# Performance work log

Measured on AMD Instinct MI355X. Metric: run time of the kernel, lower is better.

## Reference

```python
import jax, jax.numpy as jnp
import numpy as np

N = 100000      # nodes
E = 1600000     # edges (before self-loops)
F_IN = 128      # num_node_features
H = 8           # heads in conv1
C = 16          # per-head channels in conv1 (hard-coded in module)
K = 32          # num_classes (conv2 out, single head)
NEG_SLOPE = 0.2 # PyG GATConv default


def setup_inputs() -> dict:
    key = jax.random.key(0)
    ks = jax.random.split(key, 8)
    x = jax.random.normal(ks[0], (N, F_IN), dtype=jnp.float32)
    edge_index = jax.random.randint(ks[1], (2, E), 0, N, dtype=jnp.int32)
    # conv1 params (Glorot-ish scale)
    W1 = jax.random.normal(ks[2], (H * C, F_IN), dtype=jnp.float32) / np.sqrt(F_IN)
    att_src1 = jax.random.normal(ks[3], (H, C), dtype=jnp.float32) / np.sqrt(C)
    att_dst1 = jax.random.normal(ks[4], (H, C), dtype=jnp.float32) / np.sqrt(C)
    b1 = jnp.zeros((H * C,), dtype=jnp.float32)
    # conv2 params (heads=1)
    W2 = jax.random.normal(ks[5], (K, H * C), dtype=jnp.float32) / np.sqrt(H * C)
    att_src2 = jax.random.normal(ks[6], (1, K), dtype=jnp.float32) / np.sqrt(K)
    att_dst2 = jax.random.normal(ks[7], (1, K), dtype=jnp.float32) / np.sqrt(K)
    b2 = jnp.zeros((K,), dtype=jnp.float32)
    return {"inputs": x, "edge_index": edge_index,
            "W1": W1, "att_src1": att_src1, "att_dst1": att_dst1, "b1": b1,
            "W2": W2, "att_src2": att_src2, "att_dst2": att_dst2, "b2": b2}


def gat_conv(x, src, dst, W, a_src, a_dst, bias, heads, ch):
    # x: [N, F_in]; src/dst: [E2] (self-loops already appended)
    h = (x @ W.T).reshape(N, heads, ch)                  # [N, H, C]
    al_s = (h * a_src[None]).sum(-1)                     # [N, H]
    al_d = (h * a_dst[None]).sum(-1)                     # [N, H]
    e = al_s[src] + al_d[dst]                            # [E2, H]
    e = jnp.where(e >= 0, e, NEG_SLOPE * e)              # LeakyReLU
    # segment softmax over edges sharing a destination node
    m = jax.ops.segment_max(e, dst, num_segments=N)      # [N, H]
    p = jnp.exp(e - m[dst])
    s = jax.ops.segment_sum(p, dst, num_segments=N)
    alpha = p / (s[dst] + 1e-16)                         # [E2, H]
    msg = h[src] * alpha[:, :, None]                     # [E2, H, C]
    out = jax.ops.segment_sum(msg, dst, num_segments=N)  # [N, H, C]
    return out.reshape(N, heads * ch) + bias, alpha


def reference(inputs, edge_index, W1, att_src1, att_dst1, b1, W2, att_src2, att_dst2, b2):
    loop = jnp.arange(N, dtype=edge_index.dtype)
    src = jnp.concatenate([edge_index[0], loop])         # add self-loops
    dst = jnp.concatenate([edge_index[1], loop])
    x1, _ = gat_conv(inputs, src, dst, W1, att_src1, att_dst1, b1, H, C)
    x1 = jax.nn.relu(x1)                                 # [N, H*C]
    x2, alpha = gat_conv(x1, src, dst, W2, att_src2, att_dst2, b2, 1, K)
    edge_index_new = jnp.stack([src, dst])               # [2, E+N]
    return x2, edge_index_new, alpha
```

## Files before the change

kernel.cpp:

```cpp
#include <hip/hip_runtime.h>
#include <hip/hip_bf16.h>
#include <cstdint>
#include <cstddef>

#define NN  100000
#define EE  1600000
#define NE2 1700000
#define NBINS 391
#define BCAP  8192
#define EPB   16384
#define NBINBLK ((NE2 + EPB - 1) / EPB)

#define OUT_X2    3200000
#define OUT_ALPHA 6600000

__device__ __forceinline__ float lrelu(float v) { return v >= 0.f ? v : 0.2f * v; }

typedef float v2f __attribute__((ext_vector_type(2)));
typedef short short8 __attribute__((ext_vector_type(8)));
typedef float f32x4 __attribute__((ext_vector_type(4)));

__device__ __forceinline__ unsigned bf16_1(float x) {
  unsigned u = __float_as_uint(x);
  return (u + 0x7FFFu + ((u >> 16) & 1u)) >> 16;
}
__device__ __forceinline__ unsigned packbf(float lo, float hi) {
  return bf16_1(lo) | (bf16_1(hi) << 16);
}

#if __has_builtin(__builtin_amdgcn_cvt_pk_f32_fp8) && __has_builtin(__builtin_amdgcn_cvt_pk_fp8_f32)
#define HW_FP8 1
#endif

__device__ __forceinline__ float fp8dec1(unsigned b) {
  unsigned e = (b >> 3) & 15, m = b & 7;
  float v = e ? __uint_as_float(((e + 120u) << 23) | (m << 20))
              : (float)m * 0.001953125f;
  return (b & 0x80u) ? -v : v;
}
__device__ __forceinline__ unsigned fp8enc1(float x) {
  unsigned s = x < 0.f ? 0x80u : 0u;
  float a = fminf(fabsf(x), 448.f);
  if (a < 0.0009765625f) return s;
  unsigned ub = __float_as_uint(a);
  int ex = (int)(ub >> 23) - 127;
  if (ex < -6) {
    unsigned m = (unsigned)(a * 512.f + 0.5f);
    return s | (m > 7u ? 7u : m);
  }
  float sc = __uint_as_float((unsigned)(127 - ex) << 23);
  unsigned m = (unsigned)((a * sc - 1.f) * 8.f + 0.5f);
  if (m == 8u) { m = 0u; ++ex; }
  if (ex > 8) { ex = 8; m = 7u; }
  return s | ((unsigned)(ex + 7) << 3) | m;
}

template <bool HI>
__device__ __forceinline__ v2f fp8x2(unsigned u) {
#ifdef HW_FP8
  return __builtin_amdgcn_cvt_pk_f32_fp8((int)u, HI);
#else
  unsigned w = HI ? (u >> 16) : u;
  v2f r; r.x = fp8dec1(w & 255u); r.y = fp8dec1((w >> 8) & 255u);
  return r;
#endif
}
__device__ __forceinline__ unsigned packfp8x4(float a, float b, float c, float d) {
#ifdef HW_FP8
  int r = __builtin_amdgcn_cvt_pk_fp8_f32(a, b, 0, false);
  r = __builtin_amdgcn_cvt_pk_fp8_f32(c, d, r, true);
  return (unsigned)r;
#else
  return fp8enc1(a) | (fp8enc1(b) << 8) | (fp8enc1(c) << 16) | (fp8enc1(d) << 24);
#endif
}

__global__ __launch_bounds__(256) void k_gemm1(
    const float* __restrict__ x, const float* __restrict__ W1,
    const float* __restrict__ a_src, const float* __restrict__ a_dst,
    unsigned* __restrict__ h1f8, float* __restrict__ als, float* __restrict__ ald)
{
  __shared__ __align__(16) char lds[49152];
  char* xs_c = lds;
  char* Wb_c = lds + 16384;
  float* Cl  = (float*)lds;

  const int t = threadIdx.x;
  const int row0 = blockIdx.x * 64;

  #pragma unroll
  for (int i = 0; i < 16; ++i) {
    int idx4 = i * 256 + t;
    int n = idx4 >> 5, kq = idx4 & 31;
    float4 v = ((const float4*)W1)[idx4];
    unsigned lo = packbf(v.x, v.y), hi = packbf(v.z, v.w);
    int byte = n * 256 + ((((kq >> 1) ^ (n & 7)) << 4) | ((kq & 1) << 3));
    *(uint2*)(Wb_c + byte) = make_uint2(lo, hi);
  }
  #pragma unroll
  for (int i = 0; i < 8; ++i) {
    int idx4 = i * 256 + t;
    int r = idx4 >> 5, kq = idx4 & 31;
    int grow = row0 + r;
    float4 v = (grow < NN) ? ((const float4*)x)[(size_t)grow * 32 + kq]
                           : make_float4(0.f, 0.f, 0.f, 0.f);
    unsigned lo = packbf(v.x, v.y), hi = packbf(v.z, v.w);
    int byte = r * 256 + ((((kq >> 1) ^ (r & 7)) << 4) | ((kq & 1) << 3));
    *(uint2*)(xs_c + byte) = make_uint2(lo, hi);
  }
  __syncthreads();

  const int w = t >> 6, l = t & 63, m = l & 15, g = l >> 4;
  f32x4 acc[8] = {};
  const char* xrow = xs_c + (16 * w + m) * 256;
  #pragma unroll
  for (int kk = 0; kk < 4; ++kk) {
    int chunk = (((kk << 2) + g) ^ (m & 7)) << 4;
    short8 av = *(const short8*)(xrow + chunk);
    #pragma unroll
    for (int nb = 0; nb < 8; ++nb) {
      short8 bv = *(const short8*)(Wb_c + (16 * nb + m) * 256 + chunk);
      acc[nb] = __builtin_amdgcn_mfma_f32_16x16x32_bf16(av, bv, acc[nb], 0, 0, 0);
    }
  }

  __syncthreads();
  #pragma unroll
  for (int nb = 0; nb < 8; ++nb)
    #pragma unroll
    for (int j = 0; j < 4; ++j)
      Cl[(16 * w + 4 * g + j) * 128 + 16 * nb + m] = acc[nb][j];
  __syncthreads();

  const int cg = t & 31, rg = t >> 5;
  float4 sA = ((const float4*)a_src)[cg];
  float4 dA = ((const float4*)a_dst)[cg];
  #pragma unroll
  for (int j = 0; j < 8; ++j) {
    int r = 8 * rg + j;
    int grow = row0 + r;
    if (grow >= NN) break;
    float4 cv = *(const float4*)&Cl[r * 128 + 4 * cg];
    h1f8[(size_t)grow * 32 + cg] = packfp8x4(cv.x, cv.y, cv.z, cv.w);
    float ps = cv.x * sA.x + cv.y * sA.y + cv.z * sA.z + cv.w * sA.w;
    float pd = cv.x * dA.x + cv.y * dA.y + cv.z * dA.z + cv.w * dA.w;
    ps += __shfl_xor(ps, 1); ps += __shfl_xor(ps, 2);
    pd += __shfl_xor(pd, 1); pd += __shfl_xor(pd, 2);
    if ((cg & 3) == 0) {
      als[(size_t)grow * 8 + (cg >> 2)] = ps;
      ald[(size_t)grow * 8 + (cg >> 2)] = pd;
    }
  }
}

__global__ __launch_bounds__(1024) void k_bin(
    const int* __restrict__ ei, int* __restrict__ bincnt,
    unsigned* __restrict__ binbuf)
{
  __shared__ int hist[NBINS];
  __shared__ int bbase[NBINS];
  const int t = threadIdx.x;
  const int e0 = blockIdx.x * EPB;

  int mybin[16];
  unsigned mypay[16];

  for (int i = t; i < NBINS; i += 1024) hist[i] = 0;
  __syncthreads();

  #pragma unroll
  for (int k = 0; k < 16; ++k) {
    int i = e0 + k * 1024 + t;
    int b = -1; unsigned pay = 0;
    if (i < NE2) {
      int src, dst;
      if (i < EE) { src = ei[i]; dst = ei[EE + i]; } else { src = dst = i - EE; }
      b = dst >> 8;
      pay = ((unsigned)src << 8) | (dst & 255);
      atomicAdd(&hist[b], 1);
    }
    mybin[k] = b; mypay[k] = pay;
  }
  __syncthreads();

  for (int i = t; i < NBINS; i += 1024) {
    int c = hist[i];
    bbase[i] = c ? atomicAdd(&bincnt[i], c) : 0;
    hist[i] = 0;
  }
  __syncthreads();

  #pragma unroll
  for (int k = 0; k < 16; ++k) {
    int b = mybin[k];
    if (b >= 0) {
      int pos = bbase[b] + atomicAdd(&hist[b], 1);
      if (pos < BCAP) binbuf[(size_t)b * BCAP + pos] = mypay[k];
    }
  }
}

__global__ __launch_bounds__(512) void k_binscan(
    const int* __restrict__ bincnt, int* __restrict__ binstart)
{
  __shared__ int tmp[512];
  int t = threadIdx.x;
  int v = (t < NBINS) ? bincnt[t] : 0;
  tmp[t] = v;
  __syncthreads();
  #pragma unroll
  for (int off = 1; off < 512; off <<= 1) {
    int add = (t >= off) ? tmp[t - off] : 0;
    __syncthreads();
    tmp[t] += add;
    __syncthreads();
  }
  if (t < NBINS) binstart[t] = tmp[t] - v;
}

__global__ __launch_bounds__(256) void k_binsort(
    const unsigned* __restrict__ binbuf, const int* __restrict__ bincnt,
    const int* __restrict__ binstart, int* __restrict__ base,
    int* __restrict__ csr)
{
  __shared__ int deg[256];
  __shared__ int sc[256];
  __shared__ int cur[256];
  const int b = blockIdx.x;
  const int t = threadIdx.x;
  const int cnt = bincnt[b];
  const int start = binstart[b];
  const unsigned* buf = binbuf + (size_t)b * BCAP;

  deg[t] = 0;
  __syncthreads();
  for (int i = t; i < cnt; i += 256)
    atomicAdd(&deg[buf[i] & 255], 1);
  __syncthreads();

  sc[t] = deg[t];
  __syncthreads();
  #pragma unroll
  for (int off = 1; off < 256; off <<= 1) {
    int add = (t >= off) ? sc[t - off] : 0;
    __syncthreads();
    sc[t] += add;
    __syncthreads();
  }
  int excl = sc[t] - deg[t];

  int node = b * 256 + t;
  if (node < NN) base[node] = start + excl;
  if (b == NBINS - 1 && t == 0) base[NN] = NE2;
  cur[t] = excl;
  __syncthreads();

  for (int i = t; i < cnt; i += 256) {
    unsigned u = buf[i];
    int pos = atomicAdd(&cur[u & 255], 1);
    csr[start + pos] = (int)(u >> 8);
  }
}

__global__ __launch_bounds__(256) void k_node1(
    const int* __restrict__ base, const int* __restrict__ csr_src,
    const float* __restrict__ als, const float* __restrict__ ald,
    const uint2* __restrict__ h1f8, unsigned* __restrict__ acc1f8)
{
  int gid = blockIdx.x * 256 + threadIdx.x;
  int node = gid >> 4;
  int q = gid & 15;
  int h = q >> 1;
  float ad = ald[(size_t)node * 8 + h];
  int s0 = base[node], s1 = base[node + 1];
  float a0 = 0.f, a1 = 0.f, a2 = 0.f, a3 = 0.f;
  float a4 = 0.f, a5 = 0.f, a6 = 0.f, a7 = 0.f, sw = 0.f;
  int i = s0;
  int n4 = s0 + ((s1 - s0) & ~3);
  for (; i < n4; i += 4) {
    int src0 = csr_src[i + 0];
    int src1 = csr_src[i + 1];
    int src2 = csr_src[i + 2];
    int src3 = csr_src[i + 3];
    float e0 = als[(size_t)src0 * 8 + h] + ad;
    float e1 = als[(size_t)src1 * 8 + h] + ad;
    float e2 = als[(size_t)src2 * 8 + h] + ad;
    float e3 = als[(size_t)src3 * 8 + h] + ad;
    uint2 u0 = h1f8[(size_t)src0 * 16 + q];
    uint2 u1 = h1f8[(size_t)src1 * 16 + q];
    uint2 u2 = h1f8[(size_t)src2 * 16 + q];
    uint2 u3 = h1f8[(size_t)src3 * 16 + q];
    float w0 = __expf(lrelu(e0));
    float w1 = __expf(lrelu(e1));
    float w2 = __expf(lrelu(e2));
    float w3 = __expf(lrelu(e3));
    {
      v2f p0 = fp8x2<false>(u0.x), p1 = fp8x2<true>(u0.x);
      v2f p2 = fp8x2<false>(u0.y), p3 = fp8x2<true>(u0.y);
      a0 += w0 * p0.x; a1 += w0 * p0.y; a2 += w0 * p1.x; a3 += w0 * p1.y;
      a4 += w0 * p2.x; a5 += w0 * p2.y; a6 += w0 * p3.x; a7 += w0 * p3.y;
    }
    {
      v2f p0 = fp8x2<false>(u1.x), p1 = fp8x2<true>(u1.x);
      v2f p2 = fp8x2<false>(u1.y), p3 = fp8x2<true>(u1.y);
      a0 += w1 * p0.x; a1 += w1 * p0.y; a2 += w1 * p1.x; a3 += w1 * p1.y;
      a4 += w1 * p2.x; a5 += w1 * p2.y; a6 += w1 * p3.x; a7 += w1 * p3.y;
    }
    {
      v2f p0 = fp8x2<false>(u2.x), p1 = fp8x2<true>(u2.x);
      v2f p2 = fp8x2<false>(u2.y), p3 = fp8x2<true>(u2.y);
      a0 += w2 * p0.x; a1 += w2 * p0.y; a2 += w2 * p1.x; a3 += w2 * p1.y;
      a4 += w2 * p2.x; a5 += w2 * p2.y; a6 += w2 * p3.x; a7 += w2 * p3.y;
    }
    {
      v2f p0 = fp8x2<false>(u3.x), p1 = fp8x2<true>(u3.x);
      v2f p2 = fp8x2<false>(u3.y), p3 = fp8x2<true>(u3.y);
      a0 += w3 * p0.x; a1 += w3 * p0.y; a2 += w3 * p1.x; a3 += w3 * p1.y;
      a4 += w3 * p2.x; a5 += w3 * p2.y; a6 += w3 * p3.x; a7 += w3 * p3.y;
    }
    sw += w0 + w1 + w2 + w3;
  }
  for (; i < s1; ++i) {
    int src = csr_src[i];
    float w = __expf(lrelu(als[(size_t)src * 8 + h] + ad));
    uint2 u = h1f8[(size_t)src * 16 + q];
    v2f p0 = fp8x2<false>(u.x), p1 = fp8x2<true>(u.x);
    v2f p2 = fp8x2<false>(u.y), p3 = fp8x2<true>(u.y);
    a0 += w * p0.x; a1 += w * p0.y; a2 += w * p1.x; a3 += w * p1.y;
    a4 += w * p2.x; a5 += w * p2.y; a6 += w * p3.x; a7 += w * p3.y;
    sw += w;
  }
  float inv = 1.f / (sw + 1e-16f);
  ((uint2*)acc1f8)[(size_t)node * 16 + q] =
      make_uint2(packfp8x4(a0 * inv, a1 * inv, a2 * inv, a3 * inv),
                 packfp8x4(a4 * inv, a5 * inv, a6 * inv, a7 * inv));
}

__global__ __launch_bounds__(256) void k_gemm2(
    const unsigned* __restrict__ acc1f8, const float* __restrict__ b1,
    const float* __restrict__ W2, const float* __restrict__ a_src,
    const float* __restrict__ a_dst,
    unsigned* __restrict__ h2f8, float* __restrict__ als, float* __restrict__ ald)
{
  __shared__ float Wt[128 * 32];
  __shared__ float xs[64 * 132];
  const int t = threadIdx.x;
  const int row0 = blockIdx.x * 64;

  {
    const float4* W4 = (const float4*)W2;
    #pragma unroll
    for (int i = 0; i < 4; ++i) {
      int idx4 = t * 4 + i;
      int c = idx4 >> 5, f4 = idx4 & 31;
      float4 v = W4[idx4];
      Wt[(4 * f4 + 0) * 32 + c] = v.x;
      Wt[(4 * f4 + 1) * 32 + c] = v.y;
      Wt[(4 * f4 + 2) * 32 + c] = v.z;
      Wt[(4 * f4 + 3) * 32 + c] = v.w;
    }
  }
  #pragma unroll
  for (int i = 0; i < 8; ++i) {
    int idx = i * 256 + t;
    int r = idx >> 5, u = idx & 31;
    int grow = row0 + r;
    unsigned v = (grow < NN) ? acc1f8[(size_t)grow * 32 + u] : 0u;
    float4 bb = ((const float4*)b1)[u];
    v2f lo = fp8x2<false>(v), hi = fp8x2<true>(v);
    xs[r * 132 + 4 * u + 0] = fmaxf(lo.x + bb.x, 0.f);
    xs[r * 132 + 4 * u + 1] = fmaxf(lo.y + bb.y, 0.f);
    xs[r * 132 + 4 * u + 2] = fmaxf(hi.x + bb.z, 0.f);
    xs[r * 132 + 4 * u + 3] = fmaxf(hi.y + bb.w, 0.f);
  }
  __syncthreads();

  const int c4 = t & 7;
  const int rg = t >> 3;
  float acc[2][4];
  #pragma unroll
  for (int j = 0; j < 2; ++j)
    #pragma unroll
    for (int k = 0; k < 4; ++k) acc[j][k] = 0.f;

  const float4* Wt4 = (const float4*)Wt;
  #pragma unroll 4
  for (int f = 0; f < 128; ++f) {
    float4 wv = Wt4[f * 8 + c4];
    #pragma unroll
    for (int j = 0; j < 2; ++j) {
      float xv = xs[(2 * rg + j) * 132 + f];
      acc[j][0] += xv * wv.x; acc[j][1] += xv * wv.y;
      acc[j][2] += xv * wv.z; acc[j][3] += xv * wv.w;
    }
  }

  float4 sv = ((const float4*)a_src)[c4];
  float4 dv = ((const float4*)a_dst)[c4];
  #pragma unroll
  for (int j = 0; j < 2; ++j) {
    int grow = row0 + 2 * rg + j;
    if (grow < NN) {
      h2f8[(size_t)grow * 8 + c4] = packfp8x4(acc[j][0], acc[j][1], acc[j][2], acc[j][3]);
      float ps = acc[j][0] * sv.x + acc[j][1] * sv.y + acc[j][2] * sv.z + acc[j][3] * sv.w;
      float pd = acc[j][0] * dv.x + acc[j][1] * dv.y + acc[j][2] * dv.z + acc[j][3] * dv.w;
      ps += __shfl_xor(ps, 1); ps += __shfl_xor(ps, 2); ps += __shfl_xor(ps, 4);
      pd += __shfl_xor(pd, 1); pd += __shfl_xor(pd, 2); pd += __shfl_xor(pd, 4);
      if (c4 == 0) { als[grow] = ps; ald[grow] = pd; }
    }
  }
}

__global__ __launch_bounds__(256) void k_node2(
    const int* __restrict__ base, const int* __restrict__ csr_src,
    const float* __restrict__ als, const float* __restrict__ ald,
    const unsigned* __restrict__ h2f8, const float* __restrict__ b2,
    float* __restrict__ out_x2, float* __restrict__ s2)
{
  int gid = blockIdx.x * 256 + threadIdx.x;
  int node = gid >> 3, q = gid & 7;
  float ad = ald[node];
  int s0 = base[node], s1 = base[node + 1];
  float a0 = 0.f, a1 = 0.f, a2 = 0.f, a3 = 0.f, sw = 0.f;
  int i = s0;
  int n4 = s0 + ((s1 - s0) & ~3);
  for (; i < n4; i += 4) {
    int src0 = csr_src[i + 0];
    int src1 = csr_src[i + 1];
    int src2 = csr_src[i + 2];
    int src3 = csr_src[i + 3];
    float e0 = als[src0] + ad;
    float e1 = als[src1] + ad;
    float e2 = als[src2] + ad;
    float e3 = als[src3] + ad;
    unsigned u0 = h2f8[(size_t)src0 * 8 + q];
    unsigned u1 = h2f8[(size_t)src1 * 8 + q];
    unsigned u2 = h2f8[(size_t)src2 * 8 + q];
    unsigned u3 = h2f8[(size_t)src3 * 8 + q];
    float w0 = __expf(lrelu(e0));
    float w1 = __expf(lrelu(e1));
    float w2 = __expf(lrelu(e2));
    float w3 = __expf(lrelu(e3));
    { v2f lo = fp8x2<false>(u0), hi = fp8x2<true>(u0);
      a0 += w0 * lo.x; a1 += w0 * lo.y; a2 += w0 * hi.x; a3 += w0 * hi.y; }
    { v2f lo = fp8x2<false>(u1), hi = fp8x2<true>(u1);
      a0 += w1 * lo.x; a1 += w1 * lo.y; a2 += w1 * hi.x; a3 += w1 * hi.y; }
    { v2f lo = fp8x2<false>(u2), hi = fp8x2<true>(u2);
      a0 += w2 * lo.x; a1 += w2 * lo.y; a2 += w2 * hi.x; a3 += w2 * hi.y; }
    { v2f lo = fp8x2<false>(u3), hi = fp8x2<true>(u3);
      a0 += w3 * lo.x; a1 += w3 * lo.y; a2 += w3 * hi.x; a3 += w3 * hi.y; }
    sw += w0 + w1 + w2 + w3;
  }
  for (; i < s1; ++i) {
    int src = csr_src[i];
    float w = __expf(lrelu(als[src] + ad));
    unsigned u = h2f8[(size_t)src * 8 + q];
    v2f lo = fp8x2<false>(u), hi = fp8x2<true>(u);
    a0 += w * lo.x; a1 += w * lo.y; a2 += w * hi.x; a3 += w * hi.y;
    sw += w;
  }
  float inv = 1.f / (sw + 1e-16f);
  float4 bb = ((const float4*)b2)[q];
  ((float4*)out_x2)[(size_t)node * 8 + q] =
      make_float4(a0 * inv + bb.x, a1 * inv + bb.y, a2 * inv + bb.z, a3 * inv + bb.w);
  if (q == 0) s2[node] = sw;
}

__global__ __launch_bounds__(256) void k_alpha_edges(
    const int* __restrict__ ei, const float* __restrict__ als,
    const float* __restrict__ ald, const float* __restrict__ s2,
    float* __restrict__ out)
{
  int e = blockIdx.x * 256 + threadIdx.x;
  if (e >= NE2) return;
  int src, dst;
  if (e < EE) { src = ei[e]; dst = ei[EE + e]; } else { src = dst = e - EE; }
  float w = __expf(lrelu(als[src] + ald[dst]));
  out[OUT_ALPHA + e] = w / (s2[dst] + 1e-16f);
  out[OUT_X2 + e] = (float)src;
  out[OUT_X2 + NE2 + e] = (float)dst;
}

extern "C" void kernel_launch(void* const* d_in, const int* in_sizes, int n_in,
                              void* d_out, int out_size, void* d_ws, size_t ws_size,
                              hipStream_t stream)
{
  const float* x   = (const float*)d_in[0];
  const int*   ei  = (const int*)d_in[1];
  const float* W1  = (const float*)d_in[2];
  const float* as1 = (const float*)d_in[3];
  const float* ad1 = (const float*)d_in[4];
  const float* b1  = (const float*)d_in[5];
  const float* W2  = (const float*)d_in[6];
  const float* as2 = (const float*)d_in[7];
  const float* ad2 = (const float*)d_in[8];
  const float* b2  = (const float*)d_in[9];
  float* out = (float*)d_out;

  if (ws_size < 60000000) return;

  char* ws = (char*)d_ws;
  unsigned* h1f8    = (unsigned*)(ws + 0);
  unsigned* acc1f8  = (unsigned*)(ws + 12800000);
  float*    als1    = (float*)(ws + 25600000);
  float*    ald1    = (float*)(ws + 28800000);
  unsigned* h2f8    = (unsigned*)(ws + 32000000);
  float*    als2    = (float*)(ws + 35200000);
  float*    ald2    = (float*)(ws + 35600000);
  float*    s2      = (float*)(ws + 36000000);
  int*      bincnt  = (int*)(ws + 36400000);
  int*      binstart= (int*)(ws + 36404096);
  int*      base    = (int*)(ws + 36408192);
  int*      csr     = (int*)(ws + 36808208);
  unsigned* binbuf  = (unsigned*)(ws + 43608208);

  (void)hipMemsetAsync(bincnt, 0, 2048, stream);

  k_bin    <<<NBINBLK, 1024, 0, stream>>>(ei, bincnt, binbuf);
  k_binscan<<<1, 512, 0, stream>>>(bincnt, binstart);
  k_binsort<<<NBINS, 256, 0, stream>>>(binbuf, bincnt, binstart, base, csr);

  k_gemm1<<<(NN + 63) / 64, 256, 0, stream>>>(x, W1, as1, ad1, h1f8, als1, ald1);
  k_node1<<<(NN * 16) / 256, 256, 0, stream>>>(base, csr, als1, ald1,
                                               (const uint2*)h1f8, acc1f8);

  k_gemm2<<<(NN + 63) / 64, 256, 0, stream>>>(acc1f8, b1, W2, as2, ad2, h2f8, als2, ald2);
  k_node2<<<(NN * 8) / 256, 256, 0, stream>>>(base, csr, als2, ald2, h2f8, b2, out, s2);

  k_alpha_edges<<<(NE2 + 255) / 256, 256, 0, stream>>>(ei, als2, ald2, s2, out);
}
```

Before: 201.6 us.

## Split bin counters, fuse edge-index output into binning, prefetch CSR indices

Edge binning now alternates blocks between two replicas of the bin counters and bin buffers. This halves global atomic contention per counter, and the scan and sort kernels merge both replicas. The edge_index output writes move from the alpha-edge kernel into the binning kernel, which already reads the edges. The node-1 aggregation loop prefetches the next four CSR source indices, and the bf16 packing uses the hardware v_cvt_pk_bf16_f32 instruction instead of manual rounding. In exchange the workspace grows and the bin sort reads two buffers per bin.

```diff
diff --git a/kernel.cpp b/kernel.cpp
--- a/kernel.cpp
+++ b/kernel.cpp
@@ -20,12 +20,10 @@
 typedef short short8 __attribute__((ext_vector_type(8)));
 typedef float f32x4 __attribute__((ext_vector_type(4)));
 
-__device__ __forceinline__ unsigned bf16_1(float x) {
-  unsigned u = __float_as_uint(x);
-  return (u + 0x7FFFu + ((u >> 16) & 1u)) >> 16;
-}
-__device__ __forceinline__ unsigned packbf(float lo, float hi) {
-  return bf16_1(lo) | (bf16_1(hi) << 16);
+__device__ __forceinline__ unsigned cvtpk_bf16(float lo, float hi) {
+  unsigned r;
+  asm("v_cvt_pk_bf16_f32 %0, %1, %2" : "=v"(r) : "v"(lo), "v"(hi));
+  return r;
 }
 
 #if __has_builtin(__builtin_amdgcn_cvt_pk_f32_fp8) && __has_builtin(__builtin_amdgcn_cvt_pk_fp8_f32)
@@ -93,7 +91,7 @@
     int idx4 = i * 256 + t;
     int n = idx4 >> 5, kq = idx4 & 31;
     float4 v = ((const float4*)W1)[idx4];
-    unsigned lo = packbf(v.x, v.y), hi = packbf(v.z, v.w);
+    unsigned lo = cvtpk_bf16(v.x, v.y), hi = cvtpk_bf16(v.z, v.w);
     int byte = n * 256 + ((((kq >> 1) ^ (n & 7)) << 4) | ((kq & 1) << 3));
     *(uint2*)(Wb_c + byte) = make_uint2(lo, hi);
   }
@@ -104,7 +102,7 @@
     int grow = row0 + r;
     float4 v = (grow < NN) ? ((const float4*)x)[(size_t)grow * 32 + kq]
                            : make_float4(0.f, 0.f, 0.f, 0.f);
-    unsigned lo = packbf(v.x, v.y), hi = packbf(v.z, v.w);
+    unsigned lo = cvtpk_bf16(v.x, v.y), hi = cvtpk_bf16(v.z, v.w);
     int byte = r * 256 + ((((kq >> 1) ^ (r & 7)) << 4) | ((kq & 1) << 3));
     *(uint2*)(xs_c + byte) = make_uint2(lo, hi);
   }
@@ -155,12 +153,15 @@
 
 __global__ __launch_bounds__(1024) void k_bin(
     const int* __restrict__ ei, int* __restrict__ bincnt,
-    unsigned* __restrict__ binbuf)
+    unsigned* __restrict__ binbuf, float* __restrict__ out)
 {
   __shared__ int hist[NBINS];
   __shared__ int bbase[NBINS];
   const int t = threadIdx.x;
   const int e0 = blockIdx.x * EPB;
+  const int rep = blockIdx.x & 1;
+  int* bc = bincnt + rep * NBINS;
+  unsigned* bb = binbuf + (size_t)rep * NBINS * BCAP;
 
   int mybin[16];
   unsigned mypay[16];
@@ -175,6 +176,8 @@
     if (i < NE2) {
       int src, dst;
       if (i < EE) { src = ei[i]; dst = ei[EE + i]; } else { src = dst = i - EE; }
+      out[OUT_X2 + i] = (float)src;
+      out[OUT_X2 + NE2 + i] = (float)dst;
       b = dst >> 8;
       pay = ((unsigned)src << 8) | (dst & 255);
       atomicAdd(&hist[b], 1);
@@ -185,7 +188,7 @@
 
   for (int i = t; i < NBINS; i += 1024) {
     int c = hist[i];
-    bbase[i] = c ? atomicAdd(&bincnt[i], c) : 0;
+    bbase[i] = c ? atomicAdd(&bc[i], c) : 0;
     hist[i] = 0;
   }
   __syncthreads();
@@ -195,7 +198,7 @@
     int b = mybin[k];
     if (b >= 0) {
       int pos = bbase[b] + atomicAdd(&hist[b], 1);
-      if (pos < BCAP) binbuf[(size_t)b * BCAP + pos] = mypay[k];
+      if (pos < BCAP) bb[(size_t)b * BCAP + pos] = mypay[k];
     }
   }
 }
@@ -205,7 +208,7 @@
 {
   __shared__ int tmp[512];
   int t = threadIdx.x;
-  int v = (t < NBINS) ? bincnt[t] : 0;
+  int v = (t < NBINS) ? (bincnt[t] + bincnt[NBINS + t]) : 0;
   tmp[t] = v;
   __syncthreads();
   #pragma unroll
@@ -228,14 +231,16 @@
   __shared__ int cur[256];
   const int b = blockIdx.x;
   const int t = threadIdx.x;
-  const int cnt = bincnt[b];
+  const int cntA = bincnt[b];
+  const int cntB = bincnt[NBINS + b];
   const int start = binstart[b];
-  const unsigned* buf = binbuf + (size_t)b * BCAP;
+  const unsigned* bufA = binbuf + (size_t)b * BCAP;
+  const unsigned* bufB = binbuf + (size_t)(NBINS + b) * BCAP;
 
   deg[t] = 0;
   __syncthreads();
-  for (int i = t; i < cnt; i += 256)
-    atomicAdd(&deg[buf[i] & 255], 1);
+  for (int i = t; i < cntA; i += 256) atomicAdd(&deg[bufA[i] & 255], 1);
+  for (int i = t; i < cntB; i += 256) atomicAdd(&deg[bufB[i] & 255], 1);
   __syncthreads();
 
   sc[t] = deg[t];
@@ -255,8 +260,13 @@
   cur[t] = excl;
   __syncthreads();
 
-  for (int i = t; i < cnt; i += 256) {
-    unsigned u = buf[i];
+  for (int i = t; i < cntA; i += 256) {
+    unsigned u = bufA[i];
+    int pos = atomicAdd(&cur[u & 255], 1);
+    csr[start + pos] = (int)(u >> 8);
+  }
+  for (int i = t; i < cntB; i += 256) {
+    unsigned u = bufB[i];
     int pos = atomicAdd(&cur[u & 255], 1);
     csr[start + pos] = (int)(u >> 8);
   }
@@ -277,11 +287,18 @@
   float a4 = 0.f, a5 = 0.f, a6 = 0.f, a7 = 0.f, sw = 0.f;
   int i = s0;
   int n4 = s0 + ((s1 - s0) & ~3);
-  for (; i < n4; i += 4) {
-    int src0 = csr_src[i + 0];
-    int src1 = csr_src[i + 1];
-    int src2 = csr_src[i + 2];
-    int src3 = csr_src[i + 3];
+  int c0 = 0, c1 = 0, c2 = 0, c3 = 0;
+  if (i < n4) {
+    c0 = csr_src[i]; c1 = csr_src[i + 1];
+    c2 = csr_src[i + 2]; c3 = csr_src[i + 3];
+  }
+  while (i < n4) {
+    int src0 = c0, src1 = c1, src2 = c2, src3 = c3;
+    int ni = i + 4;
+    if (ni < n4) {
+      c0 = csr_src[ni]; c1 = csr_src[ni + 1];
+      c2 = csr_src[ni + 2]; c3 = csr_src[ni + 3];
+    }
     float e0 = als[(size_t)src0 * 8 + h] + ad;
     float e1 = als[(size_t)src1 * 8 + h] + ad;
     float e2 = als[(size_t)src2 * 8 + h] + ad;
@@ -319,6 +336,7 @@
       a4 += w3 * p2.x; a5 += w3 * p2.y; a6 += w3 * p3.x; a7 += w3 * p3.y;
     }
     sw += w0 + w1 + w2 + w3;
+    i = ni;
   }
   for (; i < s1; ++i) {
     int src = csr_src[i];
@@ -477,8 +495,6 @@
   if (e < EE) { src = ei[e]; dst = ei[EE + e]; } else { src = dst = e - EE; }
   float w = __expf(lrelu(als[src] + ald[dst]));
   out[OUT_ALPHA + e] = w / (s2[dst] + 1e-16f);
-  out[OUT_X2 + e] = (float)src;
-  out[OUT_X2 + NE2 + e] = (float)dst;
 }
 
 extern "C" void kernel_launch(void* const* d_in, const int* in_sizes, int n_in,
@@ -497,7 +513,7 @@
   const float* b2  = (const float*)d_in[9];
   float* out = (float*)d_out;
 
-  if (ws_size < 60000000) return;
+  if (ws_size < 70000000) return;
 
   char* ws = (char*)d_ws;
   unsigned* h1f8    = (unsigned*)(ws + 0);
@@ -514,9 +530,9 @@
   int*      csr     = (int*)(ws + 36808208);
   unsigned* binbuf  = (unsigned*)(ws + 43608208);
 
-  (void)hipMemsetAsync(bincnt, 0, 2048, stream);
-
-  k_bin    <<<NBINBLK, 1024, 0, stream>>>(ei, bincnt, binbuf);
+  (void)hipMemsetAsync(bincnt, 0, 4096, stream);
+
+  k_bin    <<<NBINBLK, 1024, 0, stream>>>(ei, bincnt, binbuf, out);
   k_binscan<<<1, 512, 0, stream>>>(bincnt, binstart);
   k_binsort<<<NBINS, 256, 0, stream>>>(binbuf, bincnt, binstart, base, csr);
 
```

Result: no change. 199.4 us (-1.1%).
